# Optimization experiments

Hardware: AMD Instinct MI355X
Metric: run time of the kernel (lower is better)

Reference implementation:

```python
import jax, jax.numpy as jnp
import numpy as np

# static model config
V, N, L, E, H, KWIN, HOPS, NCLS = 50000, 128, 64, 300, 300, 40, 3, 6
KEFF = min(KWIN, N - 1)


def _gru_dir(x, mask, Wih, Whh, bih, bhh):
    # PyTorch GRU cell (gate order r,z,n). x: [T,B,D], mask: [T,B] bool.
    # Returns per-step outputs [T,B,H], zeroed at invalid steps (pad_packed behavior).
    h0 = jnp.zeros((x.shape[1], Whh.shape[1]), x.dtype)
    def step(h, xm):
        xt, mt = xm
        gi = xt @ Wih.T + bih
        gh = h @ Whh.T + bhh
        ir, iz, inn = jnp.split(gi, 3, axis=-1)
        hr, hz, hn = jnp.split(gh, 3, axis=-1)
        r = jax.nn.sigmoid(ir + hr)
        z = jax.nn.sigmoid(iz + hz)
        n = jnp.tanh(inn + r * hn)
        hnew = (1.0 - z) * n + z * h
        hnew = jnp.where(mt[:, None], hnew, h)
        return hnew, jnp.where(mt[:, None], hnew, 0.0)
    _, out = jax.lax.scan(step, h0, (x, mask))
    return out


def _bigru(x, lens, Wih, Whh, bih, bhh):
    # variable-length bidirectional GRU, equivalent to packed nn.GRU(bidirectional=True)
    T, B, _ = x.shape
    t = jnp.arange(T)[:, None]
    mask = t < lens[None, :]
    out_f = _gru_dir(x, mask, Wih[0], Whh[0], bih[0], bhh[0])
    ridx = jnp.clip(lens[None, :] - 1 - t, 0, T - 1)  # reverse-within-length index
    x_rev = jnp.take_along_axis(x, ridx[:, :, None], axis=0)
    out_rev = _gru_dir(x_rev, mask, Wih[1], Whh[1], bih[1], bhh[1])
    out_b = jnp.where(mask[:, :, None], jnp.take_along_axis(out_rev, ridx[:, :, None], axis=0), 0.0)
    return jnp.concatenate([out_f, out_b], axis=-1)


def _att_scan(inp, gates, Wr, br, Ur, bur, Ww, bw, Uw, bu):
    # AttnGRUCell loop: hi = g*tanh(W c + r*U h) + (1-g)*h, r = sigmoid(Wr c + Ur h)
    h0 = jnp.zeros((inp.shape[1], Ur.shape[1]), inp.dtype)
    def step(h, xg):
        x, g = xg
        r = jax.nn.sigmoid(x @ Wr.T + br + h @ Ur.T + bur)
        ht = jnp.tanh(x @ Ww.T + bw + r * (h @ Uw.T + bu))
        return g * ht + (1.0 - g) * h, None
    h, _ = jax.lax.scan(step, h0, (inp, gates))
    return h


def _forward(dialogue_ids, seq_lens, emb, utt_Wih, utt_Whh, utt_bih, utt_bhh, lin_w, lin_b, ctx_Wih, ctx_Whh, ctx_bih, ctx_bhh, att_Wr_w, att_Wr_b, att_Ur_w, att_Ur_b, att_W_w, att_W_b, att_U_w, att_U_b, cls_w, cls_b):
    x = emb[dialogue_ids].transpose(1, 0, 2)  # [L,N,E]
    utt_out = _bigru(x, seq_lens, utt_Wih, utt_Whh, utt_bih, utt_bhh)  # [L,N,2H]
    max_pool = jnp.max(utt_out, axis=0)  # [N,2H]; padded steps are 0 as in pad_packed
    u = jnp.tanh(max_pool @ lin_w.T + lin_b)  # [N,H] (dropout = identity, eval mode)
    # causal context windows: for query i (1..N-1) slot k holds u[i-KEFF+k], zero-padded
    i = jnp.arange(1, N)
    k = jnp.arange(KEFF)
    idx = i[:, None] - KEFF + k[None, :]  # [N-1,KEFF]
    valid = idx >= 0
    ctx = jnp.where(valid[:, :, None], u[jnp.clip(idx, 0)], 0.0)  # [N-1,KEFF,H]
    pad_mask = ~valid  # True at zero-padded slots -> masked in attention
    ctx_t = ctx.transpose(1, 0, 2)  # [KEFF,N-1,H]
    full = jnp.full((N - 1,), KEFF)
    mem_out = _bigru(ctx_t, full, ctx_Wih, ctx_Whh, ctx_bih, ctx_bhh)  # [KEFF,N-1,2H]
    mem_fwd, mem_bwd = jnp.split(mem_out, 2, axis=-1)
    mem_bank = (ctx_t + mem_fwd + mem_bwd).transpose(1, 0, 2)  # [N-1,KEFF,H]
    query = u[1:][:, None, :]  # [N-1,1,H]
    inp = mem_bank.transpose(1, 0, 2)  # [KEFF,N-1,H]
    for hop in range(HOPS):
        attn = jnp.einsum('bqh,bkh->bqk', query, mem_bank)  # [N-1,1,KEFF]
        attn = jnp.where(pad_mask[:, None, :], -1e10, attn)
        scores = jax.nn.softmax(attn, axis=-1)
        gates = scores.transpose(2, 0, 1)  # [KEFF,N-1,1]
        h_f = _att_scan(inp, gates, att_Wr_w[hop, 0], att_Wr_b[hop, 0], att_Ur_w[hop, 0], att_Ur_b[hop, 0], att_W_w[hop, 0], att_W_b[hop, 0], att_U_w[hop, 0], att_U_b[hop, 0])
        h_b = _att_scan(inp[::-1], gates[::-1], att_Wr_w[hop, 1], att_Wr_b[hop, 1], att_Ur_w[hop, 1], att_Ur_b[hop, 1], att_W_w[hop, 1], att_W_b[hop, 1], att_U_w[hop, 1], att_U_b[hop, 1])
        attn_out = jnp.concatenate([h_f, h_b], axis=-1)[:, None, :]  # [N-1,1,2H]
        a1, a2 = jnp.split(attn_out, 2, axis=-1)
        query = query + a1 + a2
    s_context = jnp.concatenate([u[:1][:, None, :], query], axis=0)[:, 0, :]  # [N,H]
    return s_context @ cls_w.T + cls_b  # [N,NCLS]


def setup_inputs() -> dict:
    ks = jax.random.split(jax.random.key(0), 32)
    def nrm(kk, shape):
        return jax.random.normal(kk, shape, jnp.float32) * 0.05
    inp = {}
    inp['dialogue_ids'] = jax.random.randint(ks[0], (N, L), 0, V)
    inp['seq_lens'] = jax.random.randint(ks[1], (N,), 1, L + 1)
    inp['emb'] = nrm(ks[2], (V, E))
    inp['utt_Wih'] = nrm(ks[3], (2, 3 * H, E))
    inp['utt_Whh'] = nrm(ks[4], (2, 3 * H, H))
    inp['utt_bih'] = nrm(ks[5], (2, 3 * H))
    inp['utt_bhh'] = nrm(ks[6], (2, 3 * H))
    inp['lin_w'] = nrm(ks[7], (H, 2 * H))
    inp['lin_b'] = nrm(ks[8], (H,))
    inp['ctx_Wih'] = nrm(ks[9], (2, 3 * H, H))
    inp['ctx_Whh'] = nrm(ks[10], (2, 3 * H, H))
    inp['ctx_bih'] = nrm(ks[11], (2, 3 * H))
    inp['ctx_bhh'] = nrm(ks[12], (2, 3 * H))
    inp['att_Wr_w'] = nrm(ks[13], (HOPS, 2, H, H))
    inp['att_Wr_b'] = nrm(ks[14], (HOPS, 2, H))
    inp['att_Ur_w'] = nrm(ks[15], (HOPS, 2, H, H))
    inp['att_Ur_b'] = nrm(ks[16], (HOPS, 2, H))
    inp['att_W_w'] = nrm(ks[17], (HOPS, 2, H, H))
    inp['att_W_b'] = nrm(ks[18], (HOPS, 2, H))
    inp['att_U_w'] = nrm(ks[19], (HOPS, 2, H, H))
    inp['att_U_b'] = nrm(ks[20], (HOPS, 2, H))
    inp['cls_w'] = nrm(ks[21], (NCLS, H))
    inp['cls_b'] = nrm(ks[22], (NCLS,))
    return inp


def reference(dialogue_ids, seq_lens, emb, utt_Wih, utt_Whh, utt_bih, utt_bhh, lin_w, lin_b, ctx_Wih, ctx_Whh, ctx_bih, ctx_bhh, att_Wr_w, att_Wr_b, att_Ur_w, att_Ur_b, att_W_w, att_W_b, att_U_w, att_U_b, cls_w, cls_b):
    return _forward(dialogue_ids, seq_lens, emb, utt_Wih, utt_Whh, utt_bih, utt_bhh, lin_w, lin_b, ctx_Wih, ctx_Whh, ctx_bih, ctx_bhh, att_Wr_w, att_Wr_b, att_Ur_w, att_Ur_b, att_W_w, att_W_b, att_U_w, att_U_b, cls_w, cls_b)
```

## Files before the change

### kernel.cpp

```cpp
#include <hip/hip_runtime.h>

static constexpr int NN   = 128;
static constexpr int LL   = 64;
static constexpr int KWIN = 40;
static constexpr int KEFF = 40;
static constexpr int NQ   = 127;
static constexpr int NCLS = 6;
static constexpr int KP   = 320;

static constexpr int GRU_RES = 9;
static constexpr int ATT_RES = 12;
static constexpr size_t GRU_LDS = (size_t)GRU_RES * 912 * 16 + (304 + 2700) * 4;
static constexpr size_t ATT_LDS = (size_t)ATT_RES * 608 * 16 + (320 + 1216 + 304 + 40 + 40) * 4;

typedef __attribute__((ext_vector_type(8))) short short8;
typedef __attribute__((ext_vector_type(4))) float floatx4;

__device__ __forceinline__ float sigm(float x) { return 1.f / (1.f + __expf(-x)); }
__device__ __forceinline__ short f2bf(float f) {
    unsigned x = __float_as_uint(f);
    unsigned r = (x + 0x7fffu + ((x >> 16) & 1u)) >> 16;
    return (short)r;
}
__device__ __forceinline__ void bfp(unsigned v, float& lo, float& hi) {
    lo = __uint_as_float(v << 16);
    hi = __uint_as_float(v & 0xffff0000u);
}
__device__ __forceinline__ void dot8(uint4 wv, float4 h0, float4 h1, float& acc) {
    float l0, u0, l1, u1, l2, u2, l3, u3;
    bfp(wv.x, l0, u0); bfp(wv.y, l1, u1);
    bfp(wv.z, l2, u2); bfp(wv.w, l3, u3);
    acc = fmaf(l0, h0.x, acc); acc = fmaf(u0, h0.y, acc);
    acc = fmaf(l1, h0.z, acc); acc = fmaf(u1, h0.w, acc);
    acc = fmaf(l2, h1.x, acc); acc = fmaf(u2, h1.y, acc);
    acc = fmaf(l3, h1.z, acc); acc = fmaf(u3, h1.w, acc);
}

__global__ void k_gather_bf16(const float* __restrict__ emb,
                              const int* __restrict__ ids,
                              short* __restrict__ A)
{
    int r = blockIdx.x;
    int n = r & (NN - 1);
    int t = r >> 7;
    int id = ids[n * LL + t];
    int e = threadIdx.x;
    float v = (e < 300) ? emb[(size_t)id * 300 + e] : 0.f;
    A[(size_t)r * KP + e] = f2bf(v);
}

__global__ void k_conv320(const float* __restrict__ src, short* __restrict__ dst)
{
    int r = blockIdx.x, e = threadIdx.x;
    float v = (e < 300) ? src[(size_t)r * 300 + e] : 0.f;
    dst[(size_t)r * KP + e] = f2bf(v);
}

__global__ void k_pack_gru(const float* __restrict__ W, short* __restrict__ dst)
{
    int idx = blockIdx.x * 256 + threadIdx.x;
    if (idx >= 2 * 39 * 900) return;
    int u = idx % 900, dc = idx / 900;
    int c = dc % 39, d = dc / 39;
    int cs = c / 3, s = c - cs * 3;
    int p = u / 300, m = u - p * 300;
    const float* src = W + ((size_t)d * 900 + s * 300 + m) * 300 + p * 100;
    short8 sv;
#pragma unroll
    for (int i = 0; i < 8; ++i) {
        int cl = cs * 8 + i;
        sv[i] = (cl < 100) ? f2bf(src[cl]) : (short)0;
    }
    *(short8*)(dst + ((size_t)(d * 39 + c) * 912 + u) * 8) = sv;
}

__global__ void k_pack_att(const float* __restrict__ Ur, const float* __restrict__ Uw,
                           short* __restrict__ dst)
{
    int idx = blockIdx.x * 256 + threadIdx.x;
    if (idx >= 6 * 40 * 600) return;
    int u = idx % 600, hc = idx / 600;
    int c = hc % 40, hd = hc / 40;
    int cs = c >> 1, s = c & 1;
    int p = u / 300, m = u - p * 300;
    int lim = p ? 140 : 160;
    const float* src = (s ? Uw : Ur) + ((size_t)hd * 300 + m) * 300 + 160 * p;
    short8 sv;
#pragma unroll
    for (int i = 0; i < 8; ++i) {
        int cl = cs * 8 + i;
        sv[i] = (cl < lim) ? f2bf(src[cl]) : (short)0;
    }
    *(short8*)(dst + ((size_t)(hd * 40 + c) * 608 + u) * 8) = sv;
}

__global__ __launch_bounds__(256)
void k_mgemm(const short* __restrict__ A, const short* __restrict__ B,
             const float* __restrict__ bias, float* __restrict__ C,
             int R, int Cc)
{
    __shared__ short As[128 * 40];
    __shared__ short Bs[128 * 40];
    const int tid = threadIdx.x;
    const int r0 = blockIdx.y * 128, c0 = blockIdx.x * 128;
    const int w = tid >> 6, lane = tid & 63;
    const int m16 = lane & 15, quad = lane >> 4;
    const int wm = w & 1, wn = w >> 1;
    floatx4 acc[4][4];
#pragma unroll
    for (int i = 0; i < 4; ++i)
#pragma unroll
        for (int j = 0; j < 4; ++j) acc[i][j] = (floatx4){0.f, 0.f, 0.f, 0.f};

    const int ra0 = tid >> 2,         sa0 = tid & 3;
    const int ra1 = (tid + 256) >> 2, sa1 = tid & 3;

    for (int k0 = 0; k0 < KP; k0 += 32) {
        short8 za = {0,0,0,0,0,0,0,0};
        short8 a0 = za, a1 = za, b0 = za, b1 = za;
        if (r0 + ra0 < R) a0 = *(const short8*)(A + (size_t)(r0 + ra0) * KP + k0 + sa0 * 8);
        if (r0 + ra1 < R) a1 = *(const short8*)(A + (size_t)(r0 + ra1) * KP + k0 + sa1 * 8);
        if (c0 + ra0 < Cc) b0 = *(const short8*)(B + (size_t)(c0 + ra0) * KP + k0 + sa0 * 8);
        if (c0 + ra1 < Cc) b1 = *(const short8*)(B + (size_t)(c0 + ra1) * KP + k0 + sa1 * 8);
        *(short8*)(As + ra0 * 40 + sa0 * 8) = a0;
        *(short8*)(As + ra1 * 40 + sa1 * 8) = a1;
        *(short8*)(Bs + ra0 * 40 + sa0 * 8) = b0;
        *(short8*)(Bs + ra1 * 40 + sa1 * 8) = b1;
        __syncthreads();
        short8 af[4], bfr[4];
#pragma unroll
        for (int mt = 0; mt < 4; ++mt)
            af[mt] = *(const short8*)(As + (wm * 64 + mt * 16 + m16) * 40 + quad * 8);
#pragma unroll
        for (int nt = 0; nt < 4; ++nt)
            bfr[nt] = *(const short8*)(Bs + (wn * 64 + nt * 16 + m16) * 40 + quad * 8);
#pragma unroll
        for (int mt = 0; mt < 4; ++mt)
#pragma unroll
            for (int nt = 0; nt < 4; ++nt)
                acc[mt][nt] = __builtin_amdgcn_mfma_f32_16x16x32_bf16(
                    af[mt], bfr[nt], acc[mt][nt], 0, 0, 0);
        __syncthreads();
    }
#pragma unroll
    for (int mt = 0; mt < 4; ++mt) {
#pragma unroll
        for (int nt = 0; nt < 4; ++nt) {
            int col = c0 + wn * 64 + nt * 16 + m16;
            if (col >= Cc) continue;
            float bv = bias ? bias[col] : 0.f;
#pragma unroll
            for (int i = 0; i < 4; ++i) {
                int row = r0 + wm * 64 + mt * 16 + quad * 4 + i;
                if (row < R) C[(size_t)row * Cc + col] = acc[mt][nt][i] + bv;
            }
        }
    }
}

__global__ __launch_bounds__(256)
void k_gemm(const float* __restrict__ A, const float* __restrict__ B,
            const float* __restrict__ bias, float* __restrict__ C,
            int R, int Cc, int K, int actTanh)
{
    __shared__ __align__(16) float Asm[16][132];
    __shared__ __align__(16) float Bsm[16][132];
    const int tid = threadIdx.x;
    const int r0 = blockIdx.y * 128, c0 = blockIdx.x * 128;
    const int li = tid >> 1, lk = (tid & 1) * 8;
    const int tx = tid & 15, ty = tid >> 4;
    float acc[8][8];
#pragma unroll
    for (int i = 0; i < 8; ++i)
#pragma unroll
        for (int j = 0; j < 8; ++j) acc[i][j] = 0.f;
    const int nch = (K + 15) >> 4;
    for (int ch = 0; ch < nch; ++ch) {
        const int k0 = ch * 16;
        {
            float v[8];
            int gr = r0 + li, kb = k0 + lk;
            if (gr < R && kb + 8 <= K) {
                const float* p = A + (size_t)gr * K + kb;
                *(float4*)&v[0] = *(const float4*)p;
                *(float4*)&v[4] = *(const float4*)(p + 4);
            } else {
#pragma unroll
                for (int z = 0; z < 8; ++z) {
                    int k = kb + z;
                    v[z] = (gr < R && k < K) ? A[(size_t)gr * K + k] : 0.f;
                }
            }
#pragma unroll
            for (int z = 0; z < 8; ++z) Asm[lk + z][li] = v[z];
        }
        {
            float v[8];
            int gr = c0 + li, kb = k0 + lk;
            if (gr < Cc && kb + 8 <= K) {
                const float* p = B + (size_t)gr * K + kb;
                *(float4*)&v[0] = *(const float4*)p;
                *(float4*)&v[4] = *(const float4*)(p + 4);
            } else {
#pragma unroll
                for (int z = 0; z < 8; ++z) {
                    int k = kb + z;
                    v[z] = (gr < Cc && k < K) ? B[(size_t)gr * K + k] : 0.f;
                }
            }
#pragma unroll
            for (int z = 0; z < 8; ++z) Bsm[lk + z][li] = v[z];
        }
        __syncthreads();
#pragma unroll
        for (int kk = 0; kk < 16; ++kk) {
            float a[8], b[8];
            *(float4*)&a[0] = *(const float4*)&Asm[kk][ty * 8];
            *(float4*)&a[4] = *(const float4*)&Asm[kk][ty * 8 + 4];
            *(float4*)&b[0] = *(const float4*)&Bsm[kk][tx * 8];
            *(float4*)&b[4] = *(const float4*)&Bsm[kk][tx * 8 + 4];
#pragma unroll
            for (int i = 0; i < 8; ++i)
#pragma unroll
                for (int j = 0; j < 8; ++j) acc[i][j] = fmaf(a[i], b[j], acc[i][j]);
        }
        __syncthreads();
    }
#pragma unroll
    for (int i = 0; i < 8; ++i) {
        int r = r0 + ty * 8 + i;
        if (r >= R) continue;
#pragma unroll
        for (int j = 0; j < 8; ++j) {
            int c = c0 + tx * 8 + j;
            if (c >= Cc) continue;
            float v = acc[i][j];
            if (bias) v += bias[c];
            if (actTanh) v = tanhf(v);
            C[(size_t)r * Cc + c] = v;
        }
    }
}

template<bool IS_UTT>
__device__ __forceinline__ void gru_scan_body(
    const short* __restrict__ Wp,
    const float* __restrict__ bhh,
    const float* __restrict__ gi,
    int d, int chain, int NB, int len,
    float* __restrict__ outp)
{
    extern __shared__ char smem[];
    short* wlds = (short*)smem;
    float* hs   = (float*)(smem + (size_t)GRU_RES * 912 * 16);
    float* pds  = hs + 304;
    const int tid = threadIdx.x;
    const int p = tid / 300, m = tid - p * 300;
    const uint4* wall = (const uint4*)(Wp + (size_t)d * 39 * 912 * 8);
    if (tid < 912) {
#pragma unroll
        for (int c = 0; c < GRU_RES; ++c)
            *(uint4*)(wlds + ((size_t)c * 912 + tid) * 8) = wall[(size_t)c * 912 + tid];
    }
    if (tid < 304) hs[tid] = 0.f;
    float br = 0.f, bz = 0.f, bn = 0.f;
    if (tid < 300) {
        br = bhh[d * 900 + tid];
        bz = bhh[d * 900 + 300 + tid];
        bn = bhh[d * 900 + 600 + tid];
    }
    float mx = -1e30f;
    __syncthreads();
    for (int t = 0; t < len; ++t) {
        int ts = d ? (len - 1 - t) : t;
        float g0 = 0.f, g1 = 0.f, g2 = 0.f;
        if (tid < 300) {
            size_t row = ((size_t)(ts * NB + chain)) * 1800 + d * 900 + tid;
            g0 = gi[row]; g1 = gi[row + 300]; g2 = gi[row + 600];
        }
        if (tid < 900) {
            const int hb = 100 * p;
            float a0 = 0.f, a1 = 0.f, a2 = 0.f;
            uint4 ring[6];
#pragma unroll
            for (int i = 0; i < 6; ++i) ring[i] = wall[(size_t)(GRU_RES + i) * 912 + tid];
#pragma unroll
            for (int c = 0; c < GRU_RES; ++c) {
                int cs = c / 3, s = c - 3 * cs;
                float4 h0 = *(const float4*)&hs[hb + 8 * cs];
                float4 h1 = *(const float4*)&hs[hb + 8 * cs + 4];
                uint4 wv = *(const uint4*)(wlds + ((size_t)c * 912 + tid) * 8);
                if (s == 0) dot8(wv, h0, h1, a0);
                else if (s == 1) dot8(wv, h0, h1, a1);
                else dot8(wv, h0, h1, a2);
            }
#pragma unroll
            for (int i = 0; i < 39 - GRU_RES; ++i) {
                int c = GRU_RES + i, cs = c / 3, s = c - 3 * cs;
                uint4 wv = ring[i % 6];
                if (i + 6 < 39 - GRU_RES)
                    ring[i % 6] = wall[(size_t)(c + 6) * 912 + tid];
                float4 h0 = *(const float4*)&hs[hb + 8 * cs];
                float4 h1 = *(const float4*)&hs[hb + 8 * cs + 4];
                if (s == 0) dot8(wv, h0, h1, a0);
                else if (s == 1) dot8(wv, h0, h1, a1);
                else dot8(wv, h0, h1, a2);
            }
            pds[(0 * 3 + p) * 300 + m] = a0;
            pds[(1 * 3 + p) * 300 + m] = a1;
            pds[(2 * 3 + p) * 300 + m] = a2;
        }
        __syncthreads();
        if (tid < 300) {
            float dr = pds[tid] + pds[300 + tid] + pds[600 + tid] + br;
            float dz = pds[900 + tid] + pds[1200 + tid] + pds[1500 + tid] + bz;
            float dn = pds[1800 + tid] + pds[2100 + tid] + pds[2400 + tid] + bn;
            float r = sigm(g0 + dr);
            float z = sigm(g1 + dz);
            float nv = tanhf(g2 + r * dn);
            float hv = (1.f - z) * nv + z * hs[tid];
            hs[tid] = hv;
            if (IS_UTT) mx = fmaxf(mx, hv);
            else outp[(size_t)ts * 300 + tid] = hv;
        }
        __syncthreads();
    }
    if (IS_UTT && tid < 300) {
        if (len < LL) mx = fmaxf(mx, 0.f);
        outp[tid] = mx;
    }
}

__global__ __launch_bounds__(960, 1)
void k_utt_scan(const short* __restrict__ Wp, const float* __restrict__ bhh,
                const float* __restrict__ gi, const int* __restrict__ lens,
                float* __restrict__ maxpool)
{
    const int d = blockIdx.y, n = blockIdx.x;
    gru_scan_body<true>(Wp, bhh, gi, d, n, NN, lens[n],
                        maxpool + (size_t)n * 600 + d * 300);
}

__global__ __launch_bounds__(960, 1)
void k_ctx_scan(const short* __restrict__ Wp, const float* __restrict__ bhh,
                const float* __restrict__ gi, float* __restrict__ hout)
{
    const int d = blockIdx.y, q = blockIdx.x;
    gru_scan_body<false>(Wp, bhh, gi, d, q, NQ, KEFF,
                         hout + (((size_t)d * NQ + q) * KEFF) * 300);
}

__global__ void k_init_query(const float* __restrict__ u, float* __restrict__ query)
{
    int q = blockIdx.x;
    for (int e = threadIdx.x; e < 300; e += blockDim.x)
        query[(size_t)q * 300 + e] = u[(size_t)(q + 1) * 300 + e];
}

__global__ void k_build_ctxA(const float* __restrict__ u, short* __restrict__ Actx)
{
    int rkq = blockIdx.x;
    int k = rkq / NQ, q = rkq - k * NQ;
    int src = q + 1 - KWIN + k;
    int e = threadIdx.x;
    float v = (e < 300 && src >= 0) ? u[(size_t)src * 300 + e] : 0.f;
    Actx[(size_t)rkq * KP + e] = f2bf(v);
}

__global__ void k_combine(const float* __restrict__ u, const float* __restrict__ hout,
                          float* __restrict__ mem_bank, short* __restrict__ mrkq)
{
    int rkq = blockIdx.x;
    int k = rkq / NQ, q = rkq - k * NQ;
    int src = q + 1 - KWIN + k;
    int e = threadIdx.x;
    float v = 0.f;
    if (e < 300) {
        float c = (src >= 0) ? u[(size_t)src * 300 + e] : 0.f;
        v = c + hout[((size_t)q * KEFF + k) * 300 + e]
              + hout[(((size_t)NQ + q) * KEFF + k) * 300 + e];
        mem_bank[((size_t)q * KEFF + k) * 300 + e] = v;
    }
    mrkq[(size_t)rkq * KP + e] = f2bf(v);
}

__global__ __launch_bounds__(640, 1)
void k_att_scan(const short* __restrict__ Wp,
                const float* __restrict__ burb,
                const float* __restrict__ bub,
                const float* __restrict__ xgr,
                const float* __restrict__ xgw,
                const float* __restrict__ query,
                const float* __restrict__ membank,
                float* __restrict__ hbuf,
                int hop)
{
    extern __shared__ char smem[];
    short* wlds  = (short*)smem;
    float* hs    = (float*)(smem + (size_t)ATT_RES * 608 * 16);
    float* pds   = hs + 320;
    float* qv    = pds + 1216;
    float* gates = qv + 304;
    float* scr   = gates + 40;
    const int d = blockIdx.y, q = blockIdx.x, tid = threadIdx.x;
    const int hd = hop * 2 + d;
    const int p = tid / 300, m = tid - p * 300;
    const uint4* wall = (const uint4*)(Wp + (size_t)hd * 40 * 608 * 8);
    if (tid < 608) {
#pragma unroll
        for (int c = 0; c < ATT_RES; ++c)
            *(uint4*)(wlds + ((size_t)c * 608 + tid) * 8) = wall[(size_t)c * 608 + tid];
    }
    if (tid < 320) {
        hs[tid] = 0.f;
        qv[tid] = (tid < 300) ? query[(size_t)q * 300 + tid] : 0.f;
    }
    float bur = 0.f, bu = 0.f;
    if (tid < 300) { bur = burb[hd * 300 + tid]; bu = bub[hd * 300 + tid]; }
    __syncthreads();
    if (tid < 320) {
        int k = tid >> 3, part = tid & 7;
        const float* mrow = membank + ((size_t)q * KEFF + k) * 300;
        int e0 = part * 38, e1 = e0 + 38 > 300 ? 300 : e0 + 38;
        float acc = 0.f;
        for (int e = e0; e < e1; ++e) acc = fmaf(qv[e], mrow[e], acc);
        acc += __shfl_xor(acc, 1);
        acc += __shfl_xor(acc, 2);
        acc += __shfl_xor(acc, 4);
        if (part == 0) scr[k] = acc;
    }
    __syncthreads();
    if (tid < 64) {
        float s = (tid < KEFF) ? scr[tid] : -1e30f;
        if (tid < KWIN - 1 - q) s = -1e10f;
        float mxs = s;
        for (int o = 32; o > 0; o >>= 1) mxs = fmaxf(mxs, __shfl_xor(mxs, o));
        float e = (tid < KEFF) ? __expf(s - mxs) : 0.f;
        float sm = e;
        for (int o = 32; o > 0; o >>= 1) sm += __shfl_xor(sm, o);
        if (tid < KEFF) gates[tid] = e / sm;
    }
    __syncthreads();
    for (int t = 0; t < KEFF; ++t) {
        int kq = d ? (KEFF - 1 - t) : t;
        float xr = 0.f, xw = 0.f, gt = 0.f;
        if (tid < 300) {
            size_t xi = ((size_t)(kq * NQ + q)) * 1800 + (size_t)hd * 300 + tid;
            xr = xgr[xi]; xw = xgw[xi];
            gt = gates[kq];
        }
        if (tid < 600) {
            const int hb = 160 * p;
            float a0 = 0.f, a1 = 0.f;
            uint4 ring[6];
#pragma unroll
            for (int i = 0; i < 6; ++i) ring[i] = wall[(size_t)(ATT_RES + i) * 608 + tid];
#pragma unroll
            for (int c = 0; c < ATT_RES; ++c) {
                int cs = c >> 1, s = c & 1;
                float4 h0 = *(const float4*)&hs[hb + 8 * cs];
                float4 h1 = *(const float4*)&hs[hb + 8 * cs + 4];
                uint4 wv = *(const uint4*)(wlds + ((size_t)c * 608 + tid) * 8);
                if (s == 0) dot8(wv, h0, h1, a0);
                else dot8(wv, h0, h1, a1);
            }
#pragma unroll
            for (int i = 0; i < 40 - ATT_RES; ++i) {
                int c = ATT_RES + i, cs = c >> 1, s = c & 1;
                uint4 wv = ring[i % 6];
                if (i + 6 < 40 - ATT_RES)
                    ring[i % 6] = wall[(size_t)(c + 6) * 608 + tid];
                float4 h0 = *(const float4*)&hs[hb + 8 * cs];
                float4 h1 = *(const float4*)&hs[hb + 8 * cs + 4];
                if (s == 0) dot8(wv, h0, h1, a0);
                else dot8(wv, h0, h1, a1);
            }
            pds[(0 * 2 + p) * 304 + m] = a0;
            pds[(1 * 2 + p) * 304 + m] = a1;
        }
        __syncthreads();
        if (tid < 300) {
            float dr = pds[tid] + pds[304 + tid] + bur;
            float dw = pds[608 + tid] + pds[912 + tid] + bu;
            float r = sigm(xr + dr);
            float ht = tanhf(xw + r * dw);
            hs[tid] = gt * ht + (1.f - gt) * hs[tid];
        }
        __syncthreads();
    }
    if (tid < 300)
        hbuf[((size_t)d * NQ + q) * 300 + tid] = hs[tid];
}

__global__ void k_qupd(float* __restrict__ query, const float* __restrict__ hbuf)
{
    int q = blockIdx.x;
    for (int e = threadIdx.x; e < 300; e += blockDim.x)
        query[(size_t)q * 300 + e] += hbuf[(size_t)q * 300 + e]
                                    + hbuf[(size_t)(NQ + q) * 300 + e];
}

__global__ __launch_bounds__(64)
void k_cls(const float* __restrict__ u, const float* __restrict__ query,
           const float* __restrict__ cw, const float* __restrict__ cb,
           float* __restrict__ out)
{
    int n = blockIdx.x;
    const float* srow = (n == 0) ? u : (query + (size_t)(n - 1) * 300);
    int c = threadIdx.x & 7;
    int part = threadIdx.x >> 3;
    float p = 0.f;
    if (c < NCLS) {
        for (int e = part; e < 300; e += 8) p = fmaf(srow[e], cw[c * 300 + e], p);
    }
    p += __shfl_xor(p, 8);
    p += __shfl_xor(p, 16);
    p += __shfl_xor(p, 32);
    if (part == 0 && c < NCLS) out[n * NCLS + c] = p + cb[c];
}

extern "C" void kernel_launch(void* const* d_in, const int* in_sizes, int n_in,
                              void* d_out, int out_size, void* d_ws, size_t ws_size,
                              hipStream_t stream)
{
    const int* ids  = (const int*)d_in[0];
    const int* lens = (const int*)d_in[1];
    const float* emb   = (const float*)d_in[2];
    const float* uWih  = (const float*)d_in[3];
    const float* uWhh  = (const float*)d_in[4];
    const float* ubih  = (const float*)d_in[5];
    const float* ubhh  = (const float*)d_in[6];
    const float* linw  = (const float*)d_in[7];
    const float* linb  = (const float*)d_in[8];
    const float* cWih  = (const float*)d_in[9];
    const float* cWhh  = (const float*)d_in[10];
    const float* cbih  = (const float*)d_in[11];
    const float* cbhh  = (const float*)d_in[12];
    const float* aWr_w = (const float*)d_in[13];
    const float* aWr_b = (const float*)d_in[14];
    const float* aUr_w = (const float*)d_in[15];
    const float* aUr_b = (const float*)d_in[16];
    const float* aW_w  = (const float*)d_in[17];
    const float* aW_b  = (const float*)d_in[18];
    const float* aU_w  = (const float*)d_in[19];
    const float* aU_b  = (const float*)d_in[20];
    const float* clsw  = (const float*)d_in[21];
    const float* clsb  = (const float*)d_in[22];
    float* out = (float*)d_out;
    (void)in_sizes; (void)n_in; (void)out_size; (void)ws_size;

    (void)hipFuncSetAttribute((const void*)k_utt_scan,
            hipFuncAttributeMaxDynamicSharedMemorySize, (int)GRU_LDS);
    (void)hipFuncSetAttribute((const void*)k_ctx_scan,
            hipFuncAttributeMaxDynamicSharedMemorySize, (int)GRU_LDS);
    (void)hipFuncSetAttribute((const void*)k_att_scan,
            hipFuncAttributeMaxDynamicSharedMemorySize, (int)ATT_LDS);

    char* base = (char*)d_ws;
    size_t off = 0;
    auto alloc = [&](size_t b) -> void* {
        void* r = (void*)(base + off);
        off += (b + 255) & ~(size_t)255;
        return r;
    };
    short* A_utt  = (short*)alloc((size_t)8192 * KP * 2);
    float* giU    = (float*)alloc((size_t)8192 * 1800 * 4);
    float* giC    = (float*)alloc((size_t)5080 * 1800 * 4);
    short* wUihB  = (short*)alloc((size_t)1800 * KP * 2);
    short* wCihB  = (short*)alloc((size_t)1800 * KP * 2);
    short* wArB   = (short*)alloc((size_t)1800 * KP * 2);
    short* wAwB   = (short*)alloc((size_t)1800 * KP * 2);
    short* wPackU = (short*)alloc((size_t)2 * 39 * 912 * 8 * 2);
    short* wPackC = (short*)alloc((size_t)2 * 39 * 912 * 8 * 2);
    short* wPackA = (short*)alloc((size_t)6 * 40 * 608 * 8 * 2);
    short* Actx   = (short*)alloc((size_t)5080 * KP * 2);
    float* hout   = (float*)alloc((size_t)2 * NQ * KEFF * 300 * 4);
    float* membank= (float*)alloc((size_t)NQ * KEFF * 300 * 4);
    short* mrkq   = (short*)alloc((size_t)5080 * KP * 2);
    float* mpool  = (float*)alloc((size_t)NN * 600 * 4);
    float* uu     = (float*)alloc((size_t)NN * 300 * 4);
    float* query  = (float*)alloc((size_t)NQ * 300 * 4);
    float* hbuf   = (float*)alloc((size_t)2 * NQ * 300 * 4);
    float* xgr = giU;
    float* xgw = giC;

    const int RKQ = NQ * KEFF;

    k_conv320<<<dim3(1800), dim3(320), 0, stream>>>(uWih, wUihB);
    k_conv320<<<dim3(1800), dim3(320), 0, stream>>>(cWih, wCihB);
    k_conv320<<<dim3(1800), dim3(320), 0, stream>>>(aWr_w, wArB);
    k_conv320<<<dim3(1800), dim3(320), 0, stream>>>(aW_w, wAwB);
    k_pack_gru<<<dim3((2 * 39 * 900 + 255) / 256), dim3(256), 0, stream>>>(uWhh, wPackU);
    k_pack_gru<<<dim3((2 * 39 * 900 + 255) / 256), dim3(256), 0, stream>>>(cWhh, wPackC);
    k_pack_att<<<dim3((6 * 40 * 600 + 255) / 256), dim3(256), 0, stream>>>(aUr_w, aU_w, wPackA);

    k_gather_bf16<<<dim3(LL * NN), dim3(320), 0, stream>>>(emb, ids, A_utt);
    k_mgemm<<<dim3(15, 64), dim3(256), 0, stream>>>(A_utt, wUihB, ubih, giU, 8192, 1800);
    k_utt_scan<<<dim3(NN, 2), dim3(960), GRU_LDS, stream>>>(wPackU, ubhh, giU, lens, mpool);
    k_gemm<<<dim3(3, 1), dim3(256), 0, stream>>>(mpool, linw, linb, uu, NN, 300, 600, 1);
    k_init_query<<<dim3(NQ), dim3(128), 0, stream>>>(uu, query);
    k_build_ctxA<<<dim3(RKQ), dim3(320), 0, stream>>>(uu, Actx);
    k_mgemm<<<dim3(15, 40), dim3(256), 0, stream>>>(Actx, wCihB, cbih, giC, RKQ, 1800);
    k_ctx_scan<<<dim3(NQ, 2), dim3(960), GRU_LDS, stream>>>(wPackC, cbhh, giC, hout);
    k_combine<<<dim3(RKQ), dim3(320), 0, stream>>>(uu, hout, membank, mrkq);
    k_mgemm<<<dim3(15, 40), dim3(256), 0, stream>>>(mrkq, wArB, aWr_b, xgr, RKQ, 1800);
    k_mgemm<<<dim3(15, 40), dim3(256), 0, stream>>>(mrkq, wAwB, aW_b, xgw, RKQ, 1800);
    for (int hop = 0; hop < 3; ++hop) {
        k_att_scan<<<dim3(NQ, 2), dim3(640), ATT_LDS, stream>>>(
            wPackA, aUr_b, aU_b, xgr, xgw, query, membank, hbuf, hop);
        k_qupd<<<dim3(NQ), dim3(128), 0, stream>>>(query, hbuf);
    }
    k_cls<<<dim3(NN), dim3(64), 0, stream>>>(uu, query, clsw, clsb, out);
}
```

Before: 1.334 ms.

## Batch weight-prep launches, prefetch GEMM tiles, fold query init, enlarge LDS-resident weights

Merges the four bf16 weight conversions into one 2D-grid launch and the two GRU weight packs into one, and folds the query initialisation into the context-A builder, to cut kernel launch count. The MFMA GEMM now issues the next K-slice's global loads into registers before computing the current tile, overlapping load latency with compute. The number of weight chunks kept resident in LDS for the GRU and attention scans is raised, lowering per-step global weight reads at the cost of more shared memory per block. Each change is small, but together they touch several unrelated parts of the pipeline.

```diff
diff --git a/kernel.cpp b/kernel.cpp
--- a/kernel.cpp
+++ b/kernel.cpp
@@ -8,8 +8,8 @@
 static constexpr int NCLS = 6;
 static constexpr int KP   = 320;
 
-static constexpr int GRU_RES = 9;
-static constexpr int ATT_RES = 12;
+static constexpr int GRU_RES = 10;
+static constexpr int ATT_RES = 15;
 static constexpr size_t GRU_LDS = (size_t)GRU_RES * 912 * 16 + (304 + 2700) * 4;
 static constexpr size_t ATT_LDS = (size_t)ATT_RES * 608 * 16 + (320 + 1216 + 304 + 40 + 40) * 4;
 
@@ -49,15 +49,24 @@
     A[(size_t)r * KP + e] = f2bf(v);
 }
 
-__global__ void k_conv320(const float* __restrict__ src, short* __restrict__ dst)
-{
+__global__ void k_conv4(const float* __restrict__ s0, const float* __restrict__ s1,
+                        const float* __restrict__ s2, const float* __restrict__ s3,
+                        short* __restrict__ d0, short* __restrict__ d1,
+                        short* __restrict__ d2, short* __restrict__ d3)
+{
+    int which = blockIdx.y;
+    const float* s = (which == 0) ? s0 : (which == 1) ? s1 : (which == 2) ? s2 : s3;
+    short* d = (which == 0) ? d0 : (which == 1) ? d1 : (which == 2) ? d2 : d3;
     int r = blockIdx.x, e = threadIdx.x;
-    float v = (e < 300) ? src[(size_t)r * 300 + e] : 0.f;
-    dst[(size_t)r * KP + e] = f2bf(v);
-}
-
-__global__ void k_pack_gru(const float* __restrict__ W, short* __restrict__ dst)
-{
+    float v = (e < 300) ? s[(size_t)r * 300 + e] : 0.f;
+    d[(size_t)r * KP + e] = f2bf(v);
+}
+
+__global__ void k_pack_gru2(const float* __restrict__ W0, const float* __restrict__ W1,
+                            short* __restrict__ d0, short* __restrict__ d1)
+{
+    const float* W = blockIdx.y ? W1 : W0;
+    short* dst = blockIdx.y ? d1 : d0;
     int idx = blockIdx.x * 256 + threadIdx.x;
     if (idx >= 2 * 39 * 900) return;
     int u = idx % 900, dc = idx / 900;
@@ -114,19 +123,28 @@
 
     const int ra0 = tid >> 2,         sa0 = tid & 3;
     const int ra1 = (tid + 256) >> 2, sa1 = tid & 3;
-
-    for (int k0 = 0; k0 < KP; k0 += 32) {
-        short8 za = {0,0,0,0,0,0,0,0};
-        short8 a0 = za, a1 = za, b0 = za, b1 = za;
-        if (r0 + ra0 < R) a0 = *(const short8*)(A + (size_t)(r0 + ra0) * KP + k0 + sa0 * 8);
-        if (r0 + ra1 < R) a1 = *(const short8*)(A + (size_t)(r0 + ra1) * KP + k0 + sa1 * 8);
-        if (c0 + ra0 < Cc) b0 = *(const short8*)(B + (size_t)(c0 + ra0) * KP + k0 + sa0 * 8);
-        if (c0 + ra1 < Cc) b1 = *(const short8*)(B + (size_t)(c0 + ra1) * KP + k0 + sa1 * 8);
-        *(short8*)(As + ra0 * 40 + sa0 * 8) = a0;
-        *(short8*)(As + ra1 * 40 + sa1 * 8) = a1;
-        *(short8*)(Bs + ra0 * 40 + sa0 * 8) = b0;
-        *(short8*)(Bs + ra1 * 40 + sa1 * 8) = b1;
-        __syncthreads();
+    const short8 za = {0,0,0,0,0,0,0,0};
+    short8 na0 = za, na1 = za, nb0 = za, nb1 = za;
+    if (r0 + ra0 < R)  na0 = *(const short8*)(A + (size_t)(r0 + ra0) * KP + sa0 * 8);
+    if (r0 + ra1 < R)  na1 = *(const short8*)(A + (size_t)(r0 + ra1) * KP + sa1 * 8);
+    if (c0 + ra0 < Cc) nb0 = *(const short8*)(B + (size_t)(c0 + ra0) * KP + sa0 * 8);
+    if (c0 + ra1 < Cc) nb1 = *(const short8*)(B + (size_t)(c0 + ra1) * KP + sa1 * 8);
+
+#pragma unroll
+    for (int it = 0; it < KP / 32; ++it) {
+        *(short8*)(As + ra0 * 40 + sa0 * 8) = na0;
+        *(short8*)(As + ra1 * 40 + sa1 * 8) = na1;
+        *(short8*)(Bs + ra0 * 40 + sa0 * 8) = nb0;
+        *(short8*)(Bs + ra1 * 40 + sa1 * 8) = nb1;
+        __syncthreads();
+        if (it + 1 < KP / 32) {
+            const int k0 = (it + 1) * 32;
+            na0 = za; na1 = za; nb0 = za; nb1 = za;
+            if (r0 + ra0 < R)  na0 = *(const short8*)(A + (size_t)(r0 + ra0) * KP + k0 + sa0 * 8);
+            if (r0 + ra1 < R)  na1 = *(const short8*)(A + (size_t)(r0 + ra1) * KP + k0 + sa1 * 8);
+            if (c0 + ra0 < Cc) nb0 = *(const short8*)(B + (size_t)(c0 + ra0) * KP + k0 + sa0 * 8);
+            if (c0 + ra1 < Cc) nb1 = *(const short8*)(B + (size_t)(c0 + ra1) * KP + k0 + sa1 * 8);
+        }
         short8 af[4], bfr[4];
 #pragma unroll
         for (int mt = 0; mt < 4; ++mt)
@@ -350,14 +368,8 @@
                          hout + (((size_t)d * NQ + q) * KEFF) * 300);
 }
 
-__global__ void k_init_query(const float* __restrict__ u, float* __restrict__ query)
-{
-    int q = blockIdx.x;
-    for (int e = threadIdx.x; e < 300; e += blockDim.x)
-        query[(size_t)q * 300 + e] = u[(size_t)(q + 1) * 300 + e];
-}
-
-__global__ void k_build_ctxA(const float* __restrict__ u, short* __restrict__ Actx)
+__global__ void k_build_ctxA(const float* __restrict__ u, short* __restrict__ Actx,
+                             float* __restrict__ query)
 {
     int rkq = blockIdx.x;
     int k = rkq / NQ, q = rkq - k * NQ;
@@ -365,6 +377,8 @@
     int e = threadIdx.x;
     float v = (e < 300 && src >= 0) ? u[(size_t)src * 300 + e] : 0.f;
     Actx[(size_t)rkq * KP + e] = f2bf(v);
+    if (k == 0 && e < 300)
+        query[(size_t)q * 300 + e] = u[(size_t)(q + 1) * 300 + e];
 }
 
 __global__ void k_combine(const float* __restrict__ u, const float* __restrict__ hout,
@@ -586,20 +600,17 @@
 
     const int RKQ = NQ * KEFF;
 
-    k_conv320<<<dim3(1800), dim3(320), 0, stream>>>(uWih, wUihB);
-    k_conv320<<<dim3(1800), dim3(320), 0, stream>>>(cWih, wCihB);
-    k_conv320<<<dim3(1800), dim3(320), 0, stream>>>(aWr_w, wArB);
-    k_conv320<<<dim3(1800), dim3(320), 0, stream>>>(aW_w, wAwB);
-    k_pack_gru<<<dim3((2 * 39 * 900 + 255) / 256), dim3(256), 0, stream>>>(uWhh, wPackU);
-    k_pack_gru<<<dim3((2 * 39 * 900 + 255) / 256), dim3(256), 0, stream>>>(cWhh, wPackC);
+    k_conv4<<<dim3(1800, 4), dim3(320), 0, stream>>>(uWih, cWih, aWr_w, aW_w,
+                                                     wUihB, wCihB, wArB, wAwB);
+    k_pack_gru2<<<dim3((2 * 39 * 900 + 255) / 256, 2), dim3(256), 0, stream>>>(
+        uWhh, cWhh, wPackU, wPackC);
     k_pack_att<<<dim3((6 * 40 * 600 + 255) / 256), dim3(256), 0, stream>>>(aUr_w, aU_w, wPackA);
 
     k_gather_bf16<<<dim3(LL * NN), dim3(320), 0, stream>>>(emb, ids, A_utt);
     k_mgemm<<<dim3(15, 64), dim3(256), 0, stream>>>(A_utt, wUihB, ubih, giU, 8192, 1800);
     k_utt_scan<<<dim3(NN, 2), dim3(960), GRU_LDS, stream>>>(wPackU, ubhh, giU, lens, mpool);
     k_gemm<<<dim3(3, 1), dim3(256), 0, stream>>>(mpool, linw, linb, uu, NN, 300, 600, 1);
-    k_init_query<<<dim3(NQ), dim3(128), 0, stream>>>(uu, query);
-    k_build_ctxA<<<dim3(RKQ), dim3(320), 0, stream>>>(uu, Actx);
+    k_build_ctxA<<<dim3(RKQ), dim3(320), 0, stream>>>(uu, Actx, query);
     k_mgemm<<<dim3(15, 40), dim3(256), 0, stream>>>(Actx, wCihB, cbih, giC, RKQ, 1800);
     k_ctx_scan<<<dim3(NQ, 2), dim3(960), GRU_LDS, stream>>>(wPackC, cbhh, giC, hout);
     k_combine<<<dim3(RKQ), dim3(320), 0, stream>>>(uu, hout, membank, mrkq);
```

Result: faster. 1.297 ms (-2.8%).
